# Optimization experiments

Measured on AMD Instinct MI355X. Metric: run time of the kernel, lower is better.

The kernel has to match this reference:

```python
import jax, jax.numpy as jnp
import numpy as np

DIM = 256
HEADS = 8
DIM_HEAD = 32
SLICE_NUM = 64
B, N = 4, 32768


def setup_inputs() -> dict:
    key = jax.random.key(0)
    ks = jax.random.split(key, 8)
    inner = HEADS * DIM_HEAD
    s = 0.02
    x = jax.random.normal(ks[0], (B, N, DIM), dtype=jnp.float32)
    Wx = jax.random.normal(ks[1], (inner, DIM), dtype=jnp.float32) * s
    bx = jnp.zeros((inner,), dtype=jnp.float32)
    Wfx = jax.random.normal(ks[2], (inner, DIM), dtype=jnp.float32) * s
    bfx = jnp.zeros((inner,), dtype=jnp.float32)
    # orthogonal init for in_project_slice (S x D)
    g = jax.random.normal(ks[3], (SLICE_NUM, DIM_HEAD), dtype=jnp.float32)
    q, _ = jnp.linalg.qr(g.T)  # D x min(D,S); S>D so orthogonal columns
    Wslice = jnp.concatenate([q.T, jax.random.normal(ks[4], (SLICE_NUM - DIM_HEAD, DIM_HEAD)) * s], axis=0)
    bslice = jnp.zeros((SLICE_NUM,), dtype=jnp.float32)
    Wqkv = jax.random.normal(ks[5], (3 * DIM_HEAD, DIM_HEAD), dtype=jnp.float32) * s
    Wout = jax.random.normal(ks[6], (DIM, inner), dtype=jnp.float32) * s
    bout = jnp.zeros((DIM,), dtype=jnp.float32)
    temperature = jnp.ones((1, 1, HEADS, 1), dtype=jnp.float32) * 0.5
    return {"x": x, "Wx": Wx, "bx": bx, "Wfx": Wfx, "bfx": bfx,
            "Wslice": Wslice, "bslice": bslice, "Wqkv": Wqkv,
            "Wout": Wout, "bout": bout, "temperature": temperature}


def reference(x, Wx, bx, Wfx, bfx, Wslice, bslice, Wqkv, Wout, bout, temperature):
    b, n, c = x.shape
    inner = Wx.shape[0]
    d = Wqkv.shape[1]           # dim_head
    h = inner // d              # heads
    s = Wslice.shape[0]         # slice_num
    # project_input_onto_slices (irregular-mesh, standard Transolver)
    x_mid = (x @ Wx.T + bx).reshape(b, n, h, d)
    fx = (x @ Wfx.T + bfx).reshape(b, n, h, d)
    proj = jnp.einsum('bnhd,sd->bnhs', x_mid, Wslice) + bslice  # (B,N,H,S)
    # temperature-scaled softmax over slices
    temp = jnp.clip(temperature, 0.5, 5.0)  # (1,1,H,1)
    slice_weights = jax.nn.softmax(proj / temp, axis=-1)
    # pool tokens -> slice tokens
    slice_norm = slice_weights.sum(axis=1) + 0.01  # (B,H,S)
    normed = slice_weights / slice_norm[:, None, :, :]
    slice_token = jnp.einsum('bnhs,bnhd->bhsd', normed, fx)
    # small attention among slices (SDPA, scale = d^-0.5)
    qkv = jnp.einsum('bhsd,ed->bhse', slice_token, Wqkv)  # e = 3d
    q, k, v = jnp.split(qkv, 3, axis=-1)
    attn = jax.nn.softmax(jnp.einsum('bhqd,bhkd->bhqk', q, k) * (d ** -0.5), axis=-1)
    out_tok = jnp.einsum('bhqk,bhkd->bhqd', attn, v)  # (B,H,S,D)
    # unslice back to tokens
    out_x = jnp.einsum('bnhs,bhsd->bnhd', slice_weights, out_tok).reshape(b, n, inner)
    return out_x @ Wout.T + bout
```

## Files before the change

kernel.cpp:

```cpp
#include <hip/hip_runtime.h>

#define NB 4
#define NTOK 32768
#define BNT 131072
#define CDIM 256
#define HH 8
#define NCOL 768

typedef _Float16 f16;
typedef __attribute__((ext_vector_type(8))) _Float16 f16x8;
typedef __attribute__((ext_vector_type(4))) _Float16 f16x4;
typedef __attribute__((ext_vector_type(4))) float f32x4;

__device__ inline void gload_lds16(const void* g, void* l) {
    __builtin_amdgcn_global_load_lds(
        (const __attribute__((address_space(1))) void*)g,
        (__attribute__((address_space(3))) void*)l, 16, 0, 0);
}

__global__ __launch_bounds__(256) void xcvt(
    const float* __restrict__ x, f16* __restrict__ xf)
{
    long i = (long)blockIdx.x * 256 + threadIdx.x;
    const long stride = (long)gridDim.x * 256;
    const long n4 = (long)BNT * CDIM / 4;
    for (; i < n4; i += stride) {
        float4 v = ((const float4*)x)[i];
        f16x4 o = {(f16)v.x, (f16)v.y, (f16)v.z, (f16)v.w};
        *(f16x4*)(xf + i * 4) = o;
    }
}

__global__ __launch_bounds__(256) void k0_build(
    const float* __restrict__ Wx, const float* __restrict__ bx,
    const float* __restrict__ Wfx, const float* __restrict__ bfx,
    const float* __restrict__ Wslice, const float* __restrict__ bslice,
    f16* __restrict__ Bt, float* __restrict__ bcomb)
{
    int col = blockIdx.x;
    int k = threadIdx.x;
    float acc;
    if (col < 256) {
        acc = Wfx[col * 256 + k];
        if (k == 0) bcomb[col] = bfx[col];
    } else {
        int p = col - 256, h = p >> 6, s = p & 63;
        acc = 0.f;
        #pragma unroll
        for (int d = 0; d < 32; ++d)
            acc += Wx[(h * 32 + d) * 256 + k] * Wslice[s * 32 + d];
        if (k == 0) {
            float bacc = bslice[s];
            #pragma unroll
            for (int d = 0; d < 32; ++d)
                bacc += bx[h * 32 + d] * Wslice[s * 32 + d];
            bcomb[col] = bacc;
        }
    }
    Bt[(long)col * 256 + k] = (f16)acc;
}

template<int NSO, bool FUSE_SM>
__global__ __launch_bounds__(256) void gemm_f16(
    const f16* __restrict__ A, const f16* __restrict__ Bt,
    const float* __restrict__ bias, float* __restrict__ Cf,
    f16* __restrict__ Cfx, f16* __restrict__ Cw,
    const float* __restrict__ temperature, long bStrideB)
{
    constexpr int KO = NSO * 64;
    __shared__ f16 sA[128 * 64];
    __shared__ f16 sB[128 * 64];

    const int tid = threadIdx.x;
    const int lane = tid & 63;
    const int w = tid >> 6;
    const int wr = w >> 1, wc = w & 1;

    const int nx = gridDim.x;
    const int nwg = nx * gridDim.y;
    const int lid = blockIdx.y * nx + blockIdx.x;
    const int swz = (lid & 7) * (nwg >> 3) + (lid >> 3);
    const int m0 = (swz / nx) * 128, n0 = (swz % nx) * 128;

    const f16* BtB = Bt + ((long)m0 >> 15) * bStrideB;

    f32x4 acc[4][4] = {};

    for (int cs = 0; cs < NSO; ++cs) {
        __syncthreads();
        #pragma unroll
        for (int i = 0; i < 4; ++i) {
            int li = i * 256 + tid;
            int r = li >> 3, c = li & 7;
            int csrc = c ^ (r & 7);
            int lb = (i * 256 + (tid & ~63)) * 16;
            long off = cs * 64 + csrc * 8;
            gload_lds16(A + (long)(m0 + r) * KO + off, (char*)sA + lb);
            gload_lds16(BtB + (long)(n0 + r) * KO + off, (char*)sB + lb);
        }
        __syncthreads();
        #pragma unroll
        for (int ksub = 0; ksub < 2; ++ksub) {
            int cr = ksub * 4 + (lane >> 4);
            f16x8 a[4], b[4];
            #pragma unroll
            for (int mi = 0; mi < 4; ++mi) {
                int r = wr * 64 + mi * 16 + (lane & 15);
                int off = r * 128 + ((cr ^ (r & 7)) << 4);
                a[mi] = *(const f16x8*)((const char*)sA + off);
            }
            #pragma unroll
            for (int ni = 0; ni < 4; ++ni) {
                int r = wc * 64 + ni * 16 + (lane & 15);
                int off = r * 128 + ((cr ^ (r & 7)) << 4);
                b[ni] = *(const f16x8*)((const char*)sB + off);
            }
            #pragma unroll
            for (int mi = 0; mi < 4; ++mi)
                #pragma unroll
                for (int ni = 0; ni < 4; ++ni)
                    acc[mi][ni] = __builtin_amdgcn_mfma_f32_16x16x32_f16(a[mi], b[ni], acc[mi][ni], 0, 0, 0);
        }
    }
    {
        int rbase = m0 + wr * 64 + (lane >> 4) * 4;
        int cbase = n0 + wc * 64 + (lane & 15);
        float bv[4];
        #pragma unroll
        for (int ni = 0; ni < 4; ++ni) bv[ni] = bias[cbase + ni * 16];

        if constexpr (FUSE_SM) {
            bool proj = (n0 + wc * 64) >= 256;
            if (proj) {
                int h = (n0 + wc * 64 - 256) >> 6;
                float invt = 1.f / fminf(fmaxf(temperature[h], 0.5f), 5.0f);
                #pragma unroll
                for (int mi = 0; mi < 4; ++mi)
                    #pragma unroll
                    for (int rr = 0; rr < 4; ++rr) {
                        float v[4];
                        #pragma unroll
                        for (int ni = 0; ni < 4; ++ni)
                            v[ni] = (acc[mi][ni][rr] + bv[ni]) * invt;
                        float m = fmaxf(fmaxf(v[0], v[1]), fmaxf(v[2], v[3]));
                        #pragma unroll
                        for (int o = 1; o < 16; o <<= 1) m = fmaxf(m, __shfl_xor(m, o));
                        float e[4], s = 0.f;
                        #pragma unroll
                        for (int ni = 0; ni < 4; ++ni) { e[ni] = __expf(v[ni] - m); s += e[ni]; }
                        #pragma unroll
                        for (int o = 1; o < 16; o <<= 1) s += __shfl_xor(s, o);
                        float rs = 1.f / s;
                        long row = rbase + mi * 16 + rr;
                        #pragma unroll
                        for (int ni = 0; ni < 4; ++ni)
                            Cw[row * 512 + cbase + ni * 16 - 256] = (f16)(e[ni] * rs);
                    }
            } else {
                #pragma unroll
                for (int mi = 0; mi < 4; ++mi)
                    #pragma unroll
                    for (int ni = 0; ni < 4; ++ni)
                        #pragma unroll
                        for (int rr = 0; rr < 4; ++rr)
                            Cfx[(long)(rbase + mi * 16 + rr) * 256 + cbase + ni * 16] =
                                (f16)(acc[mi][ni][rr] + bv[ni]);
            }
        } else {
            #pragma unroll
            for (int mi = 0; mi < 4; ++mi)
                #pragma unroll
                for (int ni = 0; ni < 4; ++ni)
                    #pragma unroll
                    for (int rr = 0; rr < 4; ++rr)
                        Cf[(long)(rbase + mi * 16 + rr) * 256 + cbase + ni * 16] =
                            acc[mi][ni][rr] + bv[ni];
        }
    }
}

__global__ __launch_bounds__(256) void k1c_mfma(
    const f16* __restrict__ yfx, const f16* __restrict__ yw,
    float* __restrict__ partials)
{
    __shared__ char lds[36864];

    const int tid = threadIdx.x;
    const int lane = tid & 63;
    const int wv = tid >> 6;
    const int chunk64 = blockIdx.x & 63;
    const int bh = blockIdx.x >> 6;
    const int b = bh >> 3, h = bh & 7;
    const long tbase = (long)b * NTOK + (long)chunk64 * 512;

    f32x4 acc[4][3] = {};

    const f16 oe = ((lane & 15) == 0) ? (f16)1.0f : (f16)0.0f;
    const f16x8 bones = {oe, oe, oe, oe, oe, oe, oe, oe};

    const int g = lane >> 4;

    for (int iter = 0; iter < 4; ++iter) {
        const long t0 = tbase + iter * 128;
        __syncthreads();
        #pragma unroll
        for (int i = 0; i < 4; ++i) {
            int k = wv * 4 + i;
            int sc = (lane & 7) ^ ((k & 3) << 1);
            const f16* src = yw + (t0 + k * 8 + (lane >> 3)) * 512 + h * 64 + sc * 8;
            gload_lds16(src, lds + k * 1024);
        }
        #pragma unroll
        for (int i = 0; i < 2; ++i) {
            int k = wv * 2 + i;
            int tq = (k & 1) * 16 + (lane >> 2);
            int dc = (lane & 3) ^ ((tq >> 3) & 3);
            const f16* src = yfx + (t0 + k * 16 + (lane >> 2)) * 256 + h * 32 + dc * 8;
            gload_lds16(src, lds + 16384 + k * 1024);
        }
        __syncthreads();
        f16x8 a[4], bf[2];
        #pragma unroll
        for (int st = 0; st < 4; ++st) {
            int srow = st * 16 + (lane & 15);
            int schunk = (srow >> 3) ^ (g << 1);
            int base = wv * 4096 + g * 1024 + (schunk << 4) + (srow & 7) * 2;
            #pragma unroll
            for (int j = 0; j < 8; ++j)
                a[st][j] = *(const f16*)(lds + base + j * 128);
        }
        #pragma unroll
        for (int dt = 0; dt < 2; ++dt) {
            int d = dt * 16 + (lane & 15);
            int dchunk = ((d >> 3) ^ g) & 3;
            int base = 16384 + wv * 2048 + g * 512 + (dchunk << 4) + (d & 7) * 2;
            #pragma unroll
            for (int j = 0; j < 8; ++j)
                bf[dt][j] = *(const f16*)(lds + base + j * 64);
        }
        #pragma unroll
        for (int st = 0; st < 4; ++st) {
            acc[st][0] = __builtin_amdgcn_mfma_f32_16x16x32_f16(a[st], bf[0], acc[st][0], 0, 0, 0);
            acc[st][1] = __builtin_amdgcn_mfma_f32_16x16x32_f16(a[st], bf[1], acc[st][1], 0, 0, 0);
            acc[st][2] = __builtin_amdgcn_mfma_f32_16x16x32_f16(a[st], bones, acc[st][2], 0, 0, 0);
        }
    }
    __syncthreads();
    float* red = (float*)lds;
    #pragma unroll
    for (int st = 0; st < 4; ++st) {
        #pragma unroll
        for (int rr = 0; rr < 4; ++rr) {
            int s = st * 16 + g * 4 + rr;
            red[(wv * 64 + s) * 36 + (lane & 15)] = acc[st][0][rr];
            red[(wv * 64 + s) * 36 + 16 + (lane & 15)] = acc[st][1][rr];
            if ((lane & 15) == 0)
                red[(wv * 64 + s) * 36 + 32] = acc[st][2][rr];
        }
    }
    __syncthreads();
    float* P = partials + ((long)bh * 64 + chunk64) * 2112;
    for (int idx = tid; idx < 2112; idx += 256) {
        int s, c;
        if (idx < 2048) { s = idx >> 5; c = idx & 31; }
        else            { s = idx - 2048; c = 32; }
        float v = red[s * 36 + c] + red[(64 + s) * 36 + c]
                + red[(128 + s) * 36 + c] + red[(192 + s) * 36 + c];
        P[idx] = v;
    }
}

__global__ __launch_bounds__(256) void k3_slice(
    const float* __restrict__ partials,
    const float* __restrict__ Wqkv,
    const float* __restrict__ Wout,
    f16* __restrict__ OT2T)
{
    __shared__ float smem[14720];
    float* st = smem;
    float* q  = smem + 2112;
    float* kk = smem + 4224;
    float* v  = smem + 6336;
    float* L  = smem + 8448;
    float* red = L;
    float* ot = smem + 12608;

    int bh = blockIdx.x;
    int b = bh >> 3, h = bh & 7;
    int tid = threadIdx.x;

    for (int idx = tid; idx < 2112; idx += 256) {
        float s = 0.f;
        const float* P = partials + (long)bh * 64 * 2112 + idx;
        for (int c = 0; c < 64; ++c) s += P[c * 2112];
        red[idx] = s;
    }
    __syncthreads();
    for (int idx = tid; idx < 2048; idx += 256) {
        int s = idx >> 5, d = idx & 31;
        st[s * 33 + d] = red[idx] / (red[2048 + s] + 0.01f);
    }
    __syncthreads();
    for (int idx = tid; idx < 64 * 96; idx += 256) {
        int s = idx / 96, e = idx % 96;
        float acc = 0.f;
        #pragma unroll
        for (int d = 0; d < 32; ++d) acc += st[s * 33 + d] * Wqkv[e * 32 + d];
        if (e < 32)       q[s * 33 + e] = acc;
        else if (e < 64)  kk[s * 33 + (e - 32)] = acc;
        else              v[s * 33 + (e - 64)] = acc;
    }
    __syncthreads();
    for (int idx = tid; idx < 4096; idx += 256) {
        int i = idx >> 6, j = idx & 63;
        float acc = 0.f;
        #pragma unroll
        for (int d = 0; d < 32; ++d) acc += q[i * 33 + d] * kk[j * 33 + d];
        L[i * 65 + j] = acc * 0.17677669529663687f;
    }
    __syncthreads();
    {
        int lane = tid & 63, wid = tid >> 6;
        for (int r = wid; r < 64; r += 4) {
            float x = L[r * 65 + lane];
            float m = x;
            #pragma unroll
            for (int o = 32; o; o >>= 1) m = fmaxf(m, __shfl_xor(m, o));
            float e = __expf(x - m);
            float ss2 = e;
            #pragma unroll
            for (int o = 32; o; o >>= 1) ss2 += __shfl_xor(ss2, o);
            L[r * 65 + lane] = e / ss2;
        }
    }
    __syncthreads();
    for (int idx = tid; idx < 2048; idx += 256) {
        int s = idx >> 5, d = idx & 31;
        float acc = 0.f;
        #pragma unroll
        for (int j = 0; j < 64; ++j) acc += L[s * 65 + j] * v[j * 33 + d];
        ot[s * 33 + d] = acc;
    }
    __syncthreads();
    float* Wo = smem;
    for (int idx = tid; idx < 8192; idx += 256) {
        int c = idx >> 5, d = idx & 31;
        Wo[c * 33 + d] = Wout[c * 256 + h * 32 + d];
    }
    __syncthreads();
    {
        int c = tid;
        f16* O = OT2T + (long)b * 131072 + (long)c * 512 + h * 64;
        for (int s = 0; s < 64; ++s) {
            float acc = 0.f;
            #pragma unroll
            for (int d = 0; d < 32; ++d) acc += ot[s * 33 + d] * Wo[c * 33 + d];
            O[s] = (f16)acc;
        }
    }
}

extern "C" void kernel_launch(void* const* d_in, const int* in_sizes, int n_in,
                              void* d_out, int out_size, void* d_ws, size_t ws_size,
                              hipStream_t stream) {
    const float* x           = (const float*)d_in[0];
    const float* Wx          = (const float*)d_in[1];
    const float* bx          = (const float*)d_in[2];
    const float* Wfx         = (const float*)d_in[3];
    const float* bfx         = (const float*)d_in[4];
    const float* Wslice      = (const float*)d_in[5];
    const float* bslice      = (const float*)d_in[6];
    const float* Wqkv        = (const float*)d_in[7];
    const float* Wout        = (const float*)d_in[8];
    const float* bout        = (const float*)d_in[9];
    const float* temperature = (const float*)d_in[10];
    float* out = (float*)d_out;

    char* ws = (char*)d_ws;
    f16*   xf16     = (f16*)(ws);
    f16*   yfx      = (f16*)(ws + 67108864ULL);
    f16*   yw       = (f16*)(ws + 134217728ULL);
    float* partials = (float*)(ws + 268435456ULL);
    f16*   Bt       = (f16*)(ws + 285736960ULL);
    float* bcomb    = (float*)(ws + 286130176ULL);
    f16*   OT2T     = (f16*)(ws + 286133248ULL);

    k0_build<<<768, 256, 0, stream>>>(Wx, bx, Wfx, bfx, Wslice, bslice, Bt, bcomb);

    xcvt<<<2048, 256, 0, stream>>>(x, xf16);

    gemm_f16<4, true><<<dim3(NCOL / 128, BNT / 128), 256, 0, stream>>>(
        xf16, Bt, bcomb, nullptr, yfx, yw, temperature, 0L);

    k1c_mfma<<<32 * 64, 256, 0, stream>>>(yfx, yw, partials);

    k3_slice<<<32, 256, 0, stream>>>(partials, Wqkv, Wout, OT2T);

    gemm_f16<8, false><<<dim3(256 / 128, BNT / 128), 256, 0, stream>>>(
        yw, OT2T, bout, out, nullptr, nullptr, nullptr, 131072L);
}
```

Before: 382.2 us.

## Double-buffer LDS loads in GEMM and pooling kernels; stage fused epilogue stores through LDS

The f16 GEMM now uses two 32 KB LDS buffers and prefetches the next K-slice while MFMAs run on the current one. Its fused-softmax epilogue writes the tile to LDS first and then stores it to global memory as coalesced 16-byte rows. The slice-pooling kernel is also double-buffered. There each wave waits on its own loads with an explicit vmcnt and skips a block barrier, since every wave reads only the LDS region it loaded. The goal is to hide global-load latency and cut scattered 2-byte stores, at the cost of more LDS per block, which may lower occupancy.

```diff
diff --git a/kernel.cpp b/kernel.cpp
--- a/kernel.cpp
+++ b/kernel.cpp
@@ -68,8 +68,7 @@
     const float* __restrict__ temperature, long bStrideB)
 {
     constexpr int KO = NSO * 64;
-    __shared__ f16 sA[128 * 64];
-    __shared__ f16 sB[128 * 64];
+    __shared__ char lds[65536];
 
     const int tid = threadIdx.x;
     const int lane = tid & 63;
@@ -86,19 +85,28 @@
 
     f32x4 acc[4][4] = {};
 
-    for (int cs = 0; cs < NSO; ++cs) {
-        __syncthreads();
+    auto stage = [&](int cs, int buf) {
+        char* sa = lds + buf * 32768;
+        char* sb = sa + 16384;
         #pragma unroll
         for (int i = 0; i < 4; ++i) {
             int li = i * 256 + tid;
             int r = li >> 3, c = li & 7;
             int csrc = c ^ (r & 7);
             int lb = (i * 256 + (tid & ~63)) * 16;
-            long off = cs * 64 + csrc * 8;
-            gload_lds16(A + (long)(m0 + r) * KO + off, (char*)sA + lb);
-            gload_lds16(BtB + (long)(n0 + r) * KO + off, (char*)sB + lb);
-        }
-        __syncthreads();
+            long off = (long)cs * 64 + csrc * 8;
+            gload_lds16(A + (long)(m0 + r) * KO + off, sa + lb);
+            gload_lds16(BtB + (long)(n0 + r) * KO + off, sb + lb);
+        }
+    };
+
+    stage(0, 0);
+    __syncthreads();
+    for (int cs = 0; cs < NSO; ++cs) {
+        const int buf = cs & 1;
+        if (cs + 1 < NSO) stage(cs + 1, buf ^ 1);
+        const char* sa = lds + buf * 32768;
+        const char* sb = sa + 16384;
         #pragma unroll
         for (int ksub = 0; ksub < 2; ++ksub) {
             int cr = ksub * 4 + (lane >> 4);
@@ -106,14 +114,12 @@
             #pragma unroll
             for (int mi = 0; mi < 4; ++mi) {
                 int r = wr * 64 + mi * 16 + (lane & 15);
-                int off = r * 128 + ((cr ^ (r & 7)) << 4);
-                a[mi] = *(const f16x8*)((const char*)sA + off);
+                a[mi] = *(const f16x8*)(sa + r * 128 + ((cr ^ (r & 7)) << 4));
             }
             #pragma unroll
             for (int ni = 0; ni < 4; ++ni) {
                 int r = wc * 64 + ni * 16 + (lane & 15);
-                int off = r * 128 + ((cr ^ (r & 7)) << 4);
-                b[ni] = *(const f16x8*)((const char*)sB + off);
+                b[ni] = *(const f16x8*)(sb + r * 128 + ((cr ^ (r & 7)) << 4));
             }
             #pragma unroll
             for (int mi = 0; mi < 4; ++mi)
@@ -121,18 +127,20 @@
                 for (int ni = 0; ni < 4; ++ni)
                     acc[mi][ni] = __builtin_amdgcn_mfma_f32_16x16x32_f16(a[mi], b[ni], acc[mi][ni], 0, 0, 0);
         }
+        __syncthreads();
     }
     {
-        int rbase = m0 + wr * 64 + (lane >> 4) * 4;
-        int cbase = n0 + wc * 64 + (lane & 15);
+        int rloc0 = wr * 64 + (lane >> 4) * 4;
+        int cloc0 = wc * 64 + (lane & 15);
         float bv[4];
         #pragma unroll
-        for (int ni = 0; ni < 4; ++ni) bv[ni] = bias[cbase + ni * 16];
+        for (int ni = 0; ni < 4; ++ni) bv[ni] = bias[n0 + cloc0 + ni * 16];
 
         if constexpr (FUSE_SM) {
-            bool proj = (n0 + wc * 64) >= 256;
+            f16* stile = (f16*)lds;
+            bool proj = n0 >= 256;
             if (proj) {
-                int h = (n0 + wc * 64 - 256) >> 6;
+                int h = (n0 - 256 + wc * 64) >> 6;
                 float invt = 1.f / fminf(fmaxf(temperature[h], 0.5f), 5.0f);
                 #pragma unroll
                 for (int mi = 0; mi < 4; ++mi)
@@ -151,20 +159,33 @@
                         #pragma unroll
                         for (int o = 1; o < 16; o <<= 1) s += __shfl_xor(s, o);
                         float rs = 1.f / s;
-                        long row = rbase + mi * 16 + rr;
+                        int rloc = rloc0 + mi * 16 + rr;
                         #pragma unroll
                         for (int ni = 0; ni < 4; ++ni)
-                            Cw[row * 512 + cbase + ni * 16 - 256] = (f16)(e[ni] * rs);
+                            stile[rloc * 132 + cloc0 + ni * 16] = (f16)(e[ni] * rs);
                     }
             } else {
                 #pragma unroll
                 for (int mi = 0; mi < 4; ++mi)
                     #pragma unroll
-                    for (int ni = 0; ni < 4; ++ni)
-                        #pragma unroll
-                        for (int rr = 0; rr < 4; ++rr)
-                            Cfx[(long)(rbase + mi * 16 + rr) * 256 + cbase + ni * 16] =
+                    for (int rr = 0; rr < 4; ++rr) {
+                        int rloc = rloc0 + mi * 16 + rr;
+                        #pragma unroll
+                        for (int ni = 0; ni < 4; ++ni)
+                            stile[rloc * 132 + cloc0 + ni * 16] =
                                 (f16)(acc[mi][ni][rr] + bv[ni]);
+                    }
+            }
+            __syncthreads();
+            f16* dst = proj ? (Cw + (long)m0 * 512 + (n0 - 256))
+                            : (Cfx + (long)m0 * 256 + n0);
+            const int ld = proj ? 512 : 256;
+            #pragma unroll
+            for (int i = 0; i < 8; ++i) {
+                int idx = i * 256 + tid;
+                int r = idx >> 4, c = idx & 15;
+                *(f16x8*)(dst + (long)r * ld + c * 8) =
+                    *(const f16x8*)(stile + r * 132 + c * 8);
             }
         } else {
             #pragma unroll
@@ -173,7 +194,7 @@
                 for (int ni = 0; ni < 4; ++ni)
                     #pragma unroll
                     for (int rr = 0; rr < 4; ++rr)
-                        Cf[(long)(rbase + mi * 16 + rr) * 256 + cbase + ni * 16] =
+                        Cf[(long)(m0 + rloc0 + mi * 16 + rr) * 256 + n0 + cloc0 + ni * 16] =
                             acc[mi][ni][rr] + bv[ni];
         }
     }
@@ -183,7 +204,7 @@
     const f16* __restrict__ yfx, const f16* __restrict__ yw,
     float* __restrict__ partials)
 {
-    __shared__ char lds[36864];
+    __shared__ char lds[49152];
 
     const int tid = threadIdx.x;
     const int lane = tid & 63;
@@ -197,46 +218,57 @@
 
     const f16 oe = ((lane & 15) == 0) ? (f16)1.0f : (f16)0.0f;
     const f16x8 bones = {oe, oe, oe, oe, oe, oe, oe, oe};
-
     const int g = lane >> 4;
 
-    for (int iter = 0; iter < 4; ++iter) {
+    auto stage = [&](int iter, int buf) {
         const long t0 = tbase + iter * 128;
-        __syncthreads();
+        char* base = lds + buf * 24576;
         #pragma unroll
         for (int i = 0; i < 4; ++i) {
             int k = wv * 4 + i;
             int sc = (lane & 7) ^ ((k & 3) << 1);
-            const f16* src = yw + (t0 + k * 8 + (lane >> 3)) * 512 + h * 64 + sc * 8;
-            gload_lds16(src, lds + k * 1024);
+            gload_lds16(yw + (t0 + k * 8 + (lane >> 3)) * 512 + h * 64 + sc * 8,
+                        base + k * 1024);
         }
         #pragma unroll
         for (int i = 0; i < 2; ++i) {
             int k = wv * 2 + i;
             int tq = (k & 1) * 16 + (lane >> 2);
             int dc = (lane & 3) ^ ((tq >> 3) & 3);
-            const f16* src = yfx + (t0 + k * 16 + (lane >> 2)) * 256 + h * 32 + dc * 8;
-            gload_lds16(src, lds + 16384 + k * 1024);
-        }
-        __syncthreads();
+            gload_lds16(yfx + (t0 + k * 16 + (lane >> 2)) * 256 + h * 32 + dc * 8,
+                        base + 16384 + k * 1024);
+        }
+    };
+
+    stage(0, 0);
+    for (int iter = 0; iter < 4; ++iter) {
+        const int buf = iter & 1;
+        if (iter < 3) {
+            stage(iter + 1, buf ^ 1);
+            asm volatile("s_waitcnt vmcnt(6)" ::: "memory");
+        } else {
+            asm volatile("s_waitcnt vmcnt(0)" ::: "memory");
+        }
+        __builtin_amdgcn_sched_barrier(0);
+        const char* base = lds + buf * 24576;
         f16x8 a[4], bf[2];
         #pragma unroll
         for (int st = 0; st < 4; ++st) {
             int srow = st * 16 + (lane & 15);
             int schunk = (srow >> 3) ^ (g << 1);
-            int base = wv * 4096 + g * 1024 + (schunk << 4) + (srow & 7) * 2;
+            int off = wv * 4096 + g * 1024 + (schunk << 4) + (srow & 7) * 2;
             #pragma unroll
             for (int j = 0; j < 8; ++j)
-                a[st][j] = *(const f16*)(lds + base + j * 128);
+                a[st][j] = *(const f16*)(base + off + j * 128);
         }
         #pragma unroll
         for (int dt = 0; dt < 2; ++dt) {
             int d = dt * 16 + (lane & 15);
             int dchunk = ((d >> 3) ^ g) & 3;
-            int base = 16384 + wv * 2048 + g * 512 + (dchunk << 4) + (d & 7) * 2;
+            int off = 16384 + wv * 2048 + g * 512 + (dchunk << 4) + (d & 7) * 2;
             #pragma unroll
             for (int j = 0; j < 8; ++j)
-                bf[dt][j] = *(const f16*)(lds + base + j * 64);
+                bf[dt][j] = *(const f16*)(base + off + j * 64);
         }
         #pragma unroll
         for (int st = 0; st < 4; ++st) {
```

Result: no change. 375.4 us (-1.8%).
